# Kernel tuning notes

Hardware: AMD Instinct MI355X
Metric: run time of the kernel (lower is better)

## Reference

```python
import jax, jax.numpy as jnp
import numpy as np

NPOINT = 2048
RADIUS = 0.4
NSAMPLE = 32
BN_EPS = 1e-5


def setup_inputs() -> dict:
    key = jax.random.key(0)
    ks = jax.random.split(key, 6)
    B, N, C = 8, 8192, 64
    xyz = jax.random.normal(ks[0], (B, N, 3), jnp.float32)
    points = jax.random.normal(ks[1], (B, N, C), jnp.float32)
    W1 = jax.random.normal(ks[2], (3 + C, 64), jnp.float32) * 0.1
    W2 = jax.random.normal(ks[3], (64, 64), jnp.float32) * 0.1
    W3 = jax.random.normal(ks[4], (64, 128), jnp.float32) * 0.1
    return dict(
        xyz=xyz, points=points,
        W1=W1, g1=jnp.ones(64), b1=jnp.zeros(64),
        W2=W2, g2=jnp.ones(64), b2=jnp.zeros(64),
        W3=W3, g3=jnp.ones(128), b3=jnp.zeros(128),
    )


def _furthest_point_sample(xyz, npoint):
    # xyz: (B, N, 3) -> (B, npoint) int32. Sequential max-min scan, batched.
    B, N, _ = xyz.shape

    def step(carry, _):
        dists, last = carry
        p = jnp.take_along_axis(xyz, last[:, None, None], axis=1)  # (B,1,3)
        d2 = jnp.sum((xyz - p) ** 2, axis=-1)                       # (B,N)
        dists = jnp.minimum(dists, d2)
        nxt = jnp.argmax(dists, axis=-1).astype(jnp.int32)
        return (dists, nxt), nxt

    init = (jnp.full((B, N), 1e10, xyz.dtype), jnp.zeros((B,), jnp.int32))
    _, idx = jax.lax.scan(step, init, None, length=npoint - 1)      # (npoint-1, B)
    idx = jnp.concatenate([jnp.zeros((1, B), jnp.int32), idx], axis=0)
    return idx.T                                                    # (B, npoint)


def _ball_query(xyz, new_xyz, radius, nsample):
    # For each centroid take the first nsample point indices (in original order)
    # within `radius`; pad with the first found index (CUDA ball_query semantics).
    B, N, _ = xyz.shape
    d2 = jnp.sum((new_xyz[:, :, None, :] - xyz[:, None, :, :]) ** 2, axis=-1)  # (B,S,N)
    mask = d2 < radius * radius
    key = jnp.where(mask, jnp.arange(N, dtype=jnp.int32), N)
    srt = jnp.sort(key, axis=-1)[..., :nsample]                     # (B,S,K)
    first = srt[..., :1]
    first = jnp.where(first == N, 0, first)                         # empty ball -> index 0
    return jnp.where(srt == N, first, srt)


def _gather(pts, idx):
    # pts: (B,N,D), idx: (B,...) -> (B,...,D)
    return jax.vmap(lambda p, i: p[i])(pts, idx)


def reference(xyz, points, W1, g1, b1, W2, g2, b2, W3, g3, b3):
    fps_idx = _furthest_point_sample(xyz, NPOINT)                   # (B,S)
    new_xyz = _gather(xyz, fps_idx)                                 # (B,S,3)
    idx = _ball_query(xyz, new_xyz, RADIUS, NSAMPLE)                # (B,S,K)
    grouped_xyz = _gather(xyz, idx) - new_xyz[:, :, None, :]        # (B,S,K,3)
    grouped_pts = _gather(points, idx)                              # (B,S,K,C)
    feats = jnp.concatenate([grouped_xyz, grouped_pts], axis=-1)    # (B,S,K,3+C)
    for W, g, b in ((W1, g1, b1), (W2, g2, b2), (W3, g3, b3)):
        feats = feats @ W                                           # 1x1 conv
        m = feats.mean(axis=(0, 1, 2))
        v = feats.var(axis=(0, 1, 2))                               # biased, torch BN train mode
        feats = g * (feats - m) * jax.lax.rsqrt(v + BN_EPS) + b
        feats = jax.nn.relu(feats)
    new_points = feats.max(axis=2)                                  # max over nsample -> (B,S,mlp[-1])
    return new_xyz, new_points
```

## Files before the change

kernel.cpp:

```cpp
#include <hip/hip_runtime.h>

constexpr int B_ = 8, N_ = 8192, NPOINT_ = 2048, NSAMPLE_ = 32;
constexpr int M_ROWS = B_ * NPOINT_ * NSAMPLE_;
constexpr int NGROUP = B_ * NPOINT_;
constexpr size_t OFF_NXF   = 0;
constexpr size_t OFF_IDX   = 196608;
constexpr size_t OFF_WF    = 1245184;
constexpr size_t OFF_GB    = 1311488;
constexpr size_t OFF_STATS = 1313536;
constexpr size_t OFF_NP    = 1315584;
constexpr size_t OFF_FLAG  = 1317632;
constexpr size_t OFF_MAXB  = 2097152;

__device__ __forceinline__ float bf2f(unsigned short u) {
  union { unsigned u; float f; } x; x.u = ((unsigned)u) << 16; return x.f;
}
__device__ __forceinline__ float lo16f(unsigned u) {
  union { unsigned u; float f; } x; x.u = u << 16; return x.f;
}
__device__ __forceinline__ float hi16f(unsigned u) {
  union { unsigned u; float f; } x; x.u = u & 0xffff0000u; return x.f;
}
__device__ __forceinline__ unsigned short f2bf(float f) {
  union { float f; unsigned u; } x; x.f = f;
  unsigned u = x.u + 0x7FFFu + ((x.u >> 16) & 1u);
  return (unsigned short)(u >> 16);
}
__device__ __forceinline__ int f2i(float f) {
  union { float f; int i; } x; x.f = f; return x.i;
}
__device__ __forceinline__ float i2f(int i) {
  union { int i; float f; } x; x.i = i; return x.f;
}
__device__ __forceinline__ void unpack8(uint4 u, float* x) {
  x[0] = bf2f((unsigned short)(u.x & 0xffffu)); x[1] = bf2f((unsigned short)(u.x >> 16));
  x[2] = bf2f((unsigned short)(u.y & 0xffffu)); x[3] = bf2f((unsigned short)(u.y >> 16));
  x[4] = bf2f((unsigned short)(u.z & 0xffffu)); x[5] = bf2f((unsigned short)(u.z >> 16));
  x[6] = bf2f((unsigned short)(u.w & 0xffffu)); x[7] = bf2f((unsigned short)(u.w >> 16));
}
__device__ __forceinline__ float ldf(const void* p, size_t i, bool bf) {
  return bf ? bf2f(((const unsigned short*)p)[i]) : ((const float*)p)[i];
}
__device__ __forceinline__ void stf(void* p, size_t i, bool bf, float v) {
  if (bf) ((unsigned short*)p)[i] = f2bf(v);
  else    ((float*)p)[i] = v;
}

template <int CTRL>
__device__ __forceinline__ float dpp_maxf(float v) {
  int n = __builtin_amdgcn_update_dpp(0, f2i(v), CTRL, 0xF, 0xF, true);
  return fmaxf(v, i2f(n));
}

extern "C" __global__ void detect_kernel(const unsigned short* __restrict__ xyz,
                                         int* __restrict__ flag) {
  if (threadIdx.x == 0 && blockIdx.x == 0) {
    int sane = 0;
    for (int k = 0; k < 32; ++k) {
      int e = (xyz[2 * k] >> 7) & 0xff;
      if (e >= 90 && e <= 140) ++sane;
    }
    *flag = (sane >= 24) ? 1 : 0;
  }
}

extern "C" __global__ void prep_kernel(
    const void* W1, const void* W2, const void* W3,
    const void* g1, const void* b1, const void* g2, const void* b2,
    const void* g3, const void* b3,
    float* __restrict__ wf, float* __restrict__ gb, const int* __restrict__ flag) {
  const bool bf = (*flag != 0);
  int i = blockIdx.x * 256 + threadIdx.x;
  if (i < 4288)       wf[i] = ldf(W1, i, bf);
  else if (i < 8384)  wf[i] = ldf(W2, i - 4288, bf);
  else if (i < 16576) wf[i] = ldf(W3, i - 8384, bf);
  else if (i < 17088) {
    int k = i - 16576; float v;
    if (k < 64)       v = ldf(g1, k, bf);
    else if (k < 128) v = ldf(b1, k - 64, bf);
    else if (k < 192) v = ldf(g2, k - 128, bf);
    else if (k < 256) v = ldf(b2, k - 192, bf);
    else if (k < 384) v = ldf(g3, k - 256, bf);
    else              v = ldf(b3, k - 384, bf);
    gb[k] = v;
  }
}

template <bool BF>
__device__ __forceinline__ void fps_body(
    const void* xyz, void* out, float* __restrict__ nxf, float4* slots) {
#pragma clang fp contract(off)
  const int b = blockIdx.x;
  const int t = threadIdx.x;
  const int lane = t & 63, w = t >> 6;
  const size_t base = (size_t)b * N_ * 3;
  float px[8], py[8], pz[8], d[8];
  if (BF) {
    const uint4* xp = (const uint4*)((const unsigned short*)xyz + base) + t * 3;
    unsigned cc[12];
#pragma unroll
    for (int m = 0; m < 3; ++m) {
      uint4 u = xp[m];
      cc[4*m+0] = u.x; cc[4*m+1] = u.y; cc[4*m+2] = u.z; cc[4*m+3] = u.w;
    }
#pragma unroll
    for (int k = 0; k < 8; ++k) {
      if ((k & 1) == 0) {
        unsigned ra = cc[(3*k) >> 1], rb = cc[((3*k) >> 1) + 1];
        px[k] = lo16f(ra); py[k] = hi16f(ra); pz[k] = lo16f(rb);
      } else {
        unsigned ra = cc[(3*k - 1) >> 1], rb = cc[(3*k + 1) >> 1];
        px[k] = hi16f(ra); py[k] = lo16f(rb); pz[k] = hi16f(rb);
      }
    }
  } else {
#pragma unroll
    for (int k = 0; k < 8; ++k) {
      int i = t * 8 + k;
      px[k] = ((const float*)xyz)[base + i*3 + 0];
      py[k] = ((const float*)xyz)[base + i*3 + 1];
      pz[k] = ((const float*)xyz)[base + i*3 + 2];
    }
  }
#pragma unroll
  for (int k = 0; k < 8; ++k) d[k] = 1e10f;
  float s0x=0.f,s0y=0.f,s0z=0.f, s1x=0.f,s1y=0.f,s1z=0.f;
  float p0, p1, p2;
  if (BF) {
    const unsigned short* xp16 = (const unsigned short*)xyz + base;
    p0 = bf2f(xp16[0]); p1 = bf2f(xp16[1]); p2 = bf2f(xp16[2]);
  } else {
    p0 = ((const float*)xyz)[base + 0];
    p1 = ((const float*)xyz)[base + 1];
    p2 = ((const float*)xyz)[base + 2];
  }
  if (t == 0) { s0x = p0; s0y = p1; s0z = p2; }
  for (int j = 1; j < NPOINT_; ++j) {
    float bv = -1.0f;
#pragma unroll
    for (int k = 0; k < 8; ++k) {
      float dx = px[k] - p0, dy = py[k] - p1, dz = pz[k] - p2;
      float d2 = (dx*dx + dy*dy) + dz*dz;
      float dn = fminf(d[k], d2);
      d[k] = dn;
      bv = fmaxf(bv, dn);
    }
    float g = bv;
    g = dpp_maxf<0xB1>(g);
    g = dpp_maxf<0x4E>(g);
    g = dpp_maxf<0x141>(g);
    g = dpp_maxf<0x140>(g);
    g = dpp_maxf<0x142>(g);
    g = dpp_maxf<0x143>(g);
    float wmax = i2f(__builtin_amdgcn_readlane(f2i(g), 63));
    unsigned long long hm = __ballot(bv == wmax);
    int sl = (int)__builtin_ctzll(hm);
    const int pb = (j & 1) << 4;
    if (lane == sl) {
      int bk = 0;
#pragma unroll
      for (int k = 7; k >= 1; --k)
        if (d[k] == bv) bk = k;
      float cx = px[0], cy = py[0], cz = pz[0];
#pragma unroll
      for (int k = 1; k < 8; ++k)
        if (bk == k) { cx = px[k]; cy = py[k]; cz = pz[k]; }
      slots[pb + w] = make_float4(bv, cx, cy, cz);
    }
    __syncthreads();
    float4 kc = slots[pb + (lane & 15)];
    float m2 = kc.x;
    m2 = dpp_maxf<0xB1>(m2);
    m2 = dpp_maxf<0x4E>(m2);
    m2 = dpp_maxf<0x141>(m2);
    m2 = dpp_maxf<0x140>(m2);
    unsigned long long bm = __ballot(kc.x == m2);
    int s2 = (int)__builtin_ctzll(bm);
    p0 = i2f(__builtin_amdgcn_readlane(f2i(kc.y), s2));
    p1 = i2f(__builtin_amdgcn_readlane(f2i(kc.z), s2));
    p2 = i2f(__builtin_amdgcn_readlane(f2i(kc.w), s2));
    if (t == (j & 1023)) {
      if ((j >> 10) == 0) { s0x = p0; s0y = p1; s0z = p2; }
      else                { s1x = p0; s1y = p1; s1z = p2; }
    }
  }
  const bool bfrt = BF;
#pragma unroll
  for (int s = 0; s < 2; ++s) {
    float cx = (s==0)?s0x:s1x;
    float cy = (s==0)?s0y:s1y;
    float cz = (s==0)?s0z:s1z;
    size_t o = ((size_t)b * NPOINT_ + s * 1024 + t) * 3;
    nxf[o+0] = cx; nxf[o+1] = cy; nxf[o+2] = cz;
    stf(out, o+0, bfrt, cx); stf(out, o+1, bfrt, cy); stf(out, o+2, bfrt, cz);
  }
}

extern "C" __global__ void __launch_bounds__(1024, 4) fps_kernel(
    const void* xyz, void* out, float* __restrict__ nxf,
    const int* __restrict__ flag) {
  __shared__ float4 slots[32];
  if (*flag != 0) fps_body<true>(xyz, out, nxf, slots);
  else            fps_body<false>(xyz, out, nxf, slots);
}

extern "C" __global__ void __launch_bounds__(256) ballq_kernel(
    const void* xyz, const float* __restrict__ nxf,
    unsigned short* __restrict__ idxout, const int* __restrict__ flag) {
#pragma clang fp contract(off)
  const bool bf = (*flag != 0);
  const int gw = (int)((blockIdx.x * 256 + threadIdx.x) >> 6);
  const int lane = threadIdx.x & 63;
  const int b = gw >> 11;
  const int j = gw & (NPOINT_ - 1);
  const size_t base = (size_t)b * N_ * 3;
  const size_t co = ((size_t)b * NPOINT_ + j) * 3;
  const float c0 = nxf[co], c1 = nxf[co+1], c2 = nxf[co+2];
  unsigned short* out = idxout + (size_t)gw * NSAMPLE_;
  int cnt = 0, first = 0;
  for (int c = 0; c < N_/64 && cnt < NSAMPLE_; ++c) {
    int i = c * 64 + lane;
    float x = ldf(xyz, base + i*3 + 0, bf);
    float y = ldf(xyz, base + i*3 + 1, bf);
    float z = ldf(xyz, base + i*3 + 2, bf);
    float dx = x - c0, dy = y - c1, dz = z - c2;
    float d2 = (dx*dx + dy*dy) + dz*dz;
    unsigned long long m = __ballot(d2 < 0.16f);
    if (lane == 0) {
      while (m && cnt < NSAMPLE_) {
        int bit = __builtin_ctzll(m);
        int pi = c * 64 + bit;
        if (cnt == 0) first = pi;
        out[cnt] = (unsigned short)pi;
        ++cnt;
        m &= (m - 1);
      }
    }
    cnt = __shfl(cnt, 0);
  }
  first = __shfl(first, 0);
  if (lane >= cnt && lane < NSAMPLE_) out[lane] = (unsigned short)first;
}

__device__ __forceinline__ void l1_row(
    const void* xyz, const void* points, const float* __restrict__ nxf,
    const unsigned short* __restrict__ idx, const float* __restrict__ wf,
    int r, bool bf, float* acc) {
  const int b = r >> 16;
  const int j = (r >> 5) & (NPOINT_ - 1);
  const int i = idx[r];
  const size_t pt = (size_t)b * N_ + i;
  const float* cp = nxf + ((size_t)b * NPOINT_ + j) * 3;
  float f0 = ldf(xyz, pt*3 + 0, bf) - cp[0];
  float f1 = ldf(xyz, pt*3 + 1, bf) - cp[1];
  float f2 = ldf(xyz, pt*3 + 2, bf) - cp[2];
#pragma unroll
  for (int c = 0; c < 64; ++c)
    acc[c] = fmaf(f0, wf[c], fmaf(f1, wf[64+c], f2 * wf[128+c]));
  const float* wp = wf + 192;
  if (bf) {
    const uint4* pp = (const uint4*)((const unsigned short*)points + pt * 64);
#pragma unroll
    for (int s = 0; s < 8; ++s) {
      uint4 u = pp[s];
      float x[8]; unpack8(u, x);
#pragma unroll
      for (int kk = 0; kk < 8; ++kk)
#pragma unroll
        for (int c = 0; c < 64; ++c)
          acc[c] = fmaf(x[kk], wp[(s*8+kk)*64 + c], acc[c]);
    }
  } else {
    const float4* pp = (const float4*)((const float*)points + pt * 64);
#pragma unroll
    for (int s = 0; s < 16; ++s) {
      float4 u = pp[s];
      float x[4] = {u.x, u.y, u.z, u.w};
#pragma unroll
      for (int kk = 0; kk < 4; ++kk)
#pragma unroll
        for (int c = 0; c < 64; ++c)
          acc[c] = fmaf(x[kk], wp[(s*4+kk)*64 + c], acc[c]);
    }
  }
}

template <int LDW>
__device__ __forceinline__ void mm64(const float* v, const float* __restrict__ w,
                                     float* acc) {
#pragma unroll
  for (int ch = 0; ch < 64; ++ch)
#pragma unroll
    for (int c = 0; c < 64; ++c)
      acc[c] = fmaf(v[ch], w[ch*LDW + c], acc[c]);
}

__device__ __forceinline__ void bnrelu64(float* v, const float* __restrict__ np0) {
#pragma unroll
  for (int c = 0; c < 64; ++c)
    v[c] = fmaxf(fmaf(v[c], np0[c], np0[64 + c]), 0.f);
}

__device__ __forceinline__ void commit_stats64(float* a, float* __restrict__ stats) {
  float q[64];
#pragma unroll
  for (int c = 0; c < 64; ++c) q[c] = a[c] * a[c];
#pragma unroll
  for (int off = 1; off < 64; off <<= 1)
#pragma unroll
    for (int c = 0; c < 64; ++c) {
      a[c] += __shfl_xor(a[c], off);
      q[c] += __shfl_xor(q[c], off);
    }
  __shared__ float LS[4][64], LQ[4][64];
  const int t = threadIdx.x, w = t >> 6;
  if ((t & 63) == 0) {
#pragma unroll
    for (int c = 0; c < 64; ++c) { LS[w][c] = a[c]; LQ[w][c] = q[c]; }
  }
  __syncthreads();
  if (t < 64) {
    atomicAdd(&stats[t],      LS[0][t] + LS[1][t] + LS[2][t] + LS[3][t]);
    atomicAdd(&stats[64 + t], LQ[0][t] + LQ[1][t] + LQ[2][t] + LQ[3][t]);
  }
}

extern "C" __global__ void __launch_bounds__(256) p1_kernel(
    const void* xyz, const void* points, const float* __restrict__ nxf,
    const unsigned short* __restrict__ idx, const float* __restrict__ wf,
    float* __restrict__ stats, const int* __restrict__ flag) {
  const bool bf = (*flag != 0);
  const int r = blockIdx.x * 256 + threadIdx.x;
  float acc[64];
  l1_row(xyz, points, nxf, idx, wf, r, bf, acc);
  commit_stats64(acc, stats);
}

extern "C" __global__ void __launch_bounds__(256, 2) p2_kernel(
    const void* xyz, const void* points, const float* __restrict__ nxf,
    const unsigned short* __restrict__ idx, const float* __restrict__ wf,
    const float* __restrict__ w2, const float* __restrict__ np1,
    float* __restrict__ stats, const int* __restrict__ flag) {
  const bool bf = (*flag != 0);
  const int r = blockIdx.x * 256 + threadIdx.x;
  float v[64];
  l1_row(xyz, points, nxf, idx, wf, r, bf, v);
  bnrelu64(v, np1);
  float acc[64];
#pragma unroll
  for (int c = 0; c < 64; ++c) acc[c] = 0.f;
  mm64<64>(v, w2, acc);
  commit_stats64(acc, stats);
}

extern "C" __global__ void __launch_bounds__(256, 2) p3_kernel(
    const void* xyz, const void* points, const float* __restrict__ nxf,
    const unsigned short* __restrict__ idx, const float* __restrict__ wf,
    const float* __restrict__ w2, const float* __restrict__ w3,
    const float* __restrict__ np1, const float* __restrict__ np2,
    unsigned short* __restrict__ maxb, float* __restrict__ stats,
    const int* __restrict__ flag) {
  const bool bf = (*flag != 0);
  const int t = threadIdx.x, lane = t & 63, w = t >> 6;
  const int h = __builtin_amdgcn_readfirstlane(w & 1);
  const int g = blockIdx.x * 4 + (w >> 1) * 2 + (lane >> 5);
  const int r = g * 32 + (lane & 31);
  float v[64];
  l1_row(xyz, points, nxf, idx, wf, r, bf, v);
  bnrelu64(v, np1);
  float y2[64];
#pragma unroll
  for (int c = 0; c < 64; ++c) y2[c] = 0.f;
  mm64<64>(v, w2, y2);
  bnrelu64(y2, np2);
  const float* w3h = w3 + h * 64;
  float y3[64];
#pragma unroll
  for (int c = 0; c < 64; ++c) y3[c] = 0.f;
  mm64<128>(y2, w3h, y3);
  float* s = v; float* q = y2;
#pragma unroll
  for (int c = 0; c < 64; ++c) { s[c] = y3[c]; q[c] = y3[c] * y3[c]; }
#pragma unroll
  for (int off = 1; off <= 16; off <<= 1)
#pragma unroll
    for (int c = 0; c < 64; ++c)
      y3[c] = fmaxf(y3[c], __shfl_xor(y3[c], off));
  if ((lane & 31) == 0) {
    unsigned short* mo = maxb + (size_t)g * 128 + h * 64;
#pragma unroll
    for (int c = 0; c < 64; ++c) mo[c] = f2bf(y3[c]);
  }
#pragma unroll
  for (int off = 1; off < 64; off <<= 1)
#pragma unroll
    for (int c = 0; c < 64; ++c) {
      s[c] += __shfl_xor(s[c], off);
      q[c] += __shfl_xor(q[c], off);
    }
  __shared__ float LS[4][64], LQ[4][64];
  if (lane == 0) {
#pragma unroll
    for (int c = 0; c < 64; ++c) { LS[w][c] = s[c]; LQ[w][c] = q[c]; }
  }
  __syncthreads();
  if (t < 128) {
    int hh = t >> 6, cl = t & 63;
    atomicAdd(&stats[t],       LS[hh][cl] + LS[hh+2][cl]);
    atomicAdd(&stats[128 + t], LQ[hh][cl] + LQ[hh+2][cl]);
  }
}

extern "C" __global__ void nparam_kernel(
    const float* __restrict__ stats, const float* __restrict__ g,
    const float* __restrict__ bb, float* __restrict__ npar, int Cc) {
  int c = threadIdx.x;
  if (c < Cc) {
    float m = stats[c] * (1.0f / M_ROWS);
    float v = stats[Cc + c] * (1.0f / M_ROWS) - m * m;
    float sc = g[c] / sqrtf(v + 1e-5f);
    npar[c] = sc;
    npar[Cc + c] = bb[c] - m * sc;
  }
}

extern "C" __global__ void __launch_bounds__(256) final_kernel(
    const unsigned short* __restrict__ maxb, const float* __restrict__ npar,
    void* out, const int* __restrict__ flag) {
  const bool bf = (*flag != 0);
  const int gtid = blockIdx.x * 256 + threadIdx.x;
  const int c = gtid & 127;
  float y = bf2f(maxb[gtid]);
  float r = fmaxf(fmaf(y, npar[c], npar[128 + c]), 0.f);
  stf(out, (size_t)B_ * NPOINT_ * 3 + gtid, bf, r);
}

extern "C" void kernel_launch(void* const* d_in, const int* in_sizes, int n_in,
                              void* d_out, int out_size, void* d_ws, size_t ws_size,
                              hipStream_t stream) {
  const void* xyz    = d_in[0];
  const void* points = d_in[1];
  char* ws = (char*)d_ws;
  float* nxf   = (float*)(ws + OFF_NXF);
  unsigned short* wsIdx = (unsigned short*)(ws + OFF_IDX);
  float* wf    = (float*)(ws + OFF_WF);
  float* gb    = (float*)(ws + OFF_GB);
  float* stats = (float*)(ws + OFF_STATS);
  float* npar  = (float*)(ws + OFF_NP);
  int*   flag  = (int*)(ws + OFF_FLAG);
  unsigned short* maxb = (unsigned short*)(ws + OFF_MAXB);

  hipMemsetAsync(stats, 0, 512 * sizeof(float), stream);
  detect_kernel<<<1, 64, 0, stream>>>((const unsigned short*)xyz, flag);
  prep_kernel<<<67, 256, 0, stream>>>(d_in[2], d_in[5], d_in[8], d_in[3], d_in[4],
                                      d_in[6], d_in[7], d_in[9], d_in[10], wf, gb, flag);
  fps_kernel<<<B_, 1024, 0, stream>>>(xyz, d_out, nxf, flag);
  ballq_kernel<<<(B_ * NPOINT_) / 4, 256, 0, stream>>>(xyz, nxf, wsIdx, flag);
  p1_kernel<<<M_ROWS / 256, 256, 0, stream>>>(xyz, points, nxf, wsIdx, wf, stats, flag);
  nparam_kernel<<<1, 128, 0, stream>>>(stats, gb, gb + 64, npar, 64);
  p2_kernel<<<M_ROWS / 256, 256, 0, stream>>>(xyz, points, nxf, wsIdx, wf, wf + 4288,
                                              npar, stats + 128, flag);
  nparam_kernel<<<1, 128, 0, stream>>>(stats + 128, gb + 128, gb + 192, npar + 128, 64);
  p3_kernel<<<(2 * M_ROWS) / 256, 256, 0, stream>>>(xyz, points, nxf, wsIdx, wf,
                                                    wf + 4288, wf + 8384, npar,
                                                    npar + 128, maxb, stats + 256, flag);
  nparam_kernel<<<1, 128, 0, stream>>>(stats + 256, gb + 256, gb + 384, npar + 256, 128);
  final_kernel<<<(NGROUP * 128) / 256, 256, 0, stream>>>(maxb, npar + 256, d_out, flag);
}
```

Baseline: 3.982 ms.

## Use packed FP32 math in FPS and SoA xyz with parallel ballot compaction in ball query

```diff
diff --git a/kernel.cpp b/kernel.cpp
--- a/kernel.cpp
+++ b/kernel.cpp
@@ -11,6 +11,8 @@
 constexpr size_t OFF_NP    = 1315584;
 constexpr size_t OFF_FLAG  = 1317632;
 constexpr size_t OFF_MAXB  = 2097152;
+
+typedef float float2v __attribute__((ext_vector_type(2)));
 
 __device__ __forceinline__ float bf2f(unsigned short u) {
   union { unsigned u; float f; } x; x.u = ((unsigned)u) << 16; return x.f;
@@ -86,6 +88,17 @@
   }
 }
 
+extern "C" __global__ void conv_kernel(const void* xyz, float* __restrict__ sxyz,
+                                       const int* __restrict__ flag) {
+  const bool bf = (*flag != 0);
+  int i = blockIdx.x * 256 + threadIdx.x;
+  if (i < B_ * N_) {
+    sxyz[i]             = ldf(xyz, (size_t)i * 3 + 0, bf);
+    sxyz[B_*N_ + i]     = ldf(xyz, (size_t)i * 3 + 1, bf);
+    sxyz[2*B_*N_ + i]   = ldf(xyz, (size_t)i * 3 + 2, bf);
+  }
+}
+
 template <bool BF>
 __device__ __forceinline__ void fps_body(
     const void* xyz, void* out, float* __restrict__ nxf, float4* slots) {
@@ -94,7 +107,8 @@
   const int t = threadIdx.x;
   const int lane = t & 63, w = t >> 6;
   const size_t base = (size_t)b * N_ * 3;
-  float px[8], py[8], pz[8], d[8];
+  float2v px2[4], py2[4], pz2[4];
+  float d[8];
   if (BF) {
     const uint4* xp = (const uint4*)((const unsigned short*)xyz + base) + t * 3;
     unsigned cc[12];
@@ -105,21 +119,23 @@
     }
 #pragma unroll
     for (int k = 0; k < 8; ++k) {
+      float x, y, z;
       if ((k & 1) == 0) {
         unsigned ra = cc[(3*k) >> 1], rb = cc[((3*k) >> 1) + 1];
-        px[k] = lo16f(ra); py[k] = hi16f(ra); pz[k] = lo16f(rb);
+        x = lo16f(ra); y = hi16f(ra); z = lo16f(rb);
       } else {
         unsigned ra = cc[(3*k - 1) >> 1], rb = cc[(3*k + 1) >> 1];
-        px[k] = hi16f(ra); py[k] = lo16f(rb); pz[k] = hi16f(rb);
+        x = hi16f(ra); y = lo16f(rb); z = hi16f(rb);
       }
+      px2[k >> 1][k & 1] = x; py2[k >> 1][k & 1] = y; pz2[k >> 1][k & 1] = z;
     }
   } else {
 #pragma unroll
     for (int k = 0; k < 8; ++k) {
       int i = t * 8 + k;
-      px[k] = ((const float*)xyz)[base + i*3 + 0];
-      py[k] = ((const float*)xyz)[base + i*3 + 1];
-      pz[k] = ((const float*)xyz)[base + i*3 + 2];
+      px2[k >> 1][k & 1] = ((const float*)xyz)[base + i*3 + 0];
+      py2[k >> 1][k & 1] = ((const float*)xyz)[base + i*3 + 1];
+      pz2[k >> 1][k & 1] = ((const float*)xyz)[base + i*3 + 2];
     }
   }
 #pragma unroll
@@ -136,14 +152,24 @@
   }
   if (t == 0) { s0x = p0; s0y = p1; s0z = p2; }
   for (int j = 1; j < NPOINT_; ++j) {
+    float2v n0, n1, n2;
+    n0[0] = -p0; n0[1] = -p0;
+    n1[0] = -p1; n1[1] = -p1;
+    n2[0] = -p2; n2[1] = -p2;
     float bv = -1.0f;
 #pragma unroll
-    for (int k = 0; k < 8; ++k) {
-      float dx = px[k] - p0, dy = py[k] - p1, dz = pz[k] - p2;
-      float d2 = (dx*dx + dy*dy) + dz*dz;
-      float dn = fminf(d[k], d2);
-      d[k] = dn;
-      bv = fmaxf(bv, dn);
+    for (int p = 0; p < 4; ++p) {
+      float2v dx, dy, dz, qx, qy, qz, ts, dv;
+      asm("v_pk_add_f32 %0, %1, %2" : "=v"(dx) : "v"(px2[p]), "v"(n0));
+      asm("v_pk_add_f32 %0, %1, %2" : "=v"(dy) : "v"(py2[p]), "v"(n1));
+      asm("v_pk_add_f32 %0, %1, %2" : "=v"(dz) : "v"(pz2[p]), "v"(n2));
+      asm("v_pk_mul_f32 %0, %1, %1" : "=v"(qx) : "v"(dx));
+      asm("v_pk_mul_f32 %0, %1, %1" : "=v"(qy) : "v"(dy));
+      asm("v_pk_mul_f32 %0, %1, %1" : "=v"(qz) : "v"(dz));
+      asm("v_pk_add_f32 %0, %1, %2" : "=v"(ts) : "v"(qx), "v"(qy));
+      asm("v_pk_add_f32 %0, %1, %2" : "=v"(dv) : "v"(ts), "v"(qz));
+      float dn0 = fminf(d[2*p],   dv[0]); d[2*p]   = dn0; bv = fmaxf(bv, dn0);
+      float dn1 = fminf(d[2*p+1], dv[1]); d[2*p+1] = dn1; bv = fmaxf(bv, dn1);
     }
     float g = bv;
     g = dpp_maxf<0xB1>(g);
@@ -161,10 +187,10 @@
 #pragma unroll
       for (int k = 7; k >= 1; --k)
         if (d[k] == bv) bk = k;
-      float cx = px[0], cy = py[0], cz = pz[0];
+      float cx = px2[0][0], cy = py2[0][0], cz = pz2[0][0];
 #pragma unroll
       for (int k = 1; k < 8; ++k)
-        if (bk == k) { cx = px[k]; cy = py[k]; cz = pz[k]; }
+        if (bk == k) { cx = px2[k>>1][k&1]; cy = py2[k>>1][k&1]; cz = pz2[k>>1][k&1]; }
       slots[pb + w] = make_float4(bv, cx, cy, cz);
     }
     __syncthreads();
@@ -205,41 +231,42 @@
 }
 
 extern "C" __global__ void __launch_bounds__(256) ballq_kernel(
-    const void* xyz, const float* __restrict__ nxf,
-    unsigned short* __restrict__ idxout, const int* __restrict__ flag) {
+    const float* __restrict__ sxyz, const float* __restrict__ nxf,
+    unsigned short* __restrict__ idxout) {
 #pragma clang fp contract(off)
-  const bool bf = (*flag != 0);
   const int gw = (int)((blockIdx.x * 256 + threadIdx.x) >> 6);
   const int lane = threadIdx.x & 63;
   const int b = gw >> 11;
   const int j = gw & (NPOINT_ - 1);
-  const size_t base = (size_t)b * N_ * 3;
+  const float* sx = sxyz;
+  const float* sy = sxyz + B_ * N_;
+  const float* sz = sxyz + 2 * B_ * N_;
+  const size_t pbase = (size_t)b * N_;
   const size_t co = ((size_t)b * NPOINT_ + j) * 3;
   const float c0 = nxf[co], c1 = nxf[co+1], c2 = nxf[co+2];
   unsigned short* out = idxout + (size_t)gw * NSAMPLE_;
-  int cnt = 0, first = 0;
+  int cnt = 0, first = -1;
   for (int c = 0; c < N_/64 && cnt < NSAMPLE_; ++c) {
     int i = c * 64 + lane;
-    float x = ldf(xyz, base + i*3 + 0, bf);
-    float y = ldf(xyz, base + i*3 + 1, bf);
-    float z = ldf(xyz, base + i*3 + 2, bf);
-    float dx = x - c0, dy = y - c1, dz = z - c2;
+    float dx = sx[pbase + i] - c0;
+    float dy = sy[pbase + i] - c1;
+    float dz = sz[pbase + i] - c2;
     float d2 = (dx*dx + dy*dy) + dz*dz;
-    unsigned long long m = __ballot(d2 < 0.16f);
-    if (lane == 0) {
-      while (m && cnt < NSAMPLE_) {
-        int bit = __builtin_ctzll(m);
-        int pi = c * 64 + bit;
-        if (cnt == 0) first = pi;
-        out[cnt] = (unsigned short)pi;
-        ++cnt;
-        m &= (m - 1);
+    bool hit = d2 < 0.16f;
+    unsigned long long m = __ballot(hit);
+    if (m) {
+      if (first < 0) first = c * 64 + (int)__builtin_ctzll(m);
+      int rank = __builtin_amdgcn_mbcnt_hi(
+          (unsigned)(m >> 32), __builtin_amdgcn_mbcnt_lo((unsigned)m, 0));
+      if (hit) {
+        int pos = cnt + rank;
+        if (pos < NSAMPLE_) out[pos] = (unsigned short)i;
       }
-    }
-    cnt = __shfl(cnt, 0);
-  }
-  first = __shfl(first, 0);
-  if (lane >= cnt && lane < NSAMPLE_) out[lane] = (unsigned short)first;
+      cnt += __builtin_popcountll(m);
+    }
+  }
+  if (first < 0) first = 0;
+  if (lane < NSAMPLE_ && lane >= cnt) out[lane] = (unsigned short)first;
 }
 
 __device__ __forceinline__ void l1_row(
@@ -449,13 +476,15 @@
   float* npar  = (float*)(ws + OFF_NP);
   int*   flag  = (int*)(ws + OFF_FLAG);
   unsigned short* maxb = (unsigned short*)(ws + OFF_MAXB);
+  float* sxyz  = (float*)(ws + OFF_MAXB);
 
   hipMemsetAsync(stats, 0, 512 * sizeof(float), stream);
   detect_kernel<<<1, 64, 0, stream>>>((const unsigned short*)xyz, flag);
   prep_kernel<<<67, 256, 0, stream>>>(d_in[2], d_in[5], d_in[8], d_in[3], d_in[4],
                                       d_in[6], d_in[7], d_in[9], d_in[10], wf, gb, flag);
+  conv_kernel<<<(B_ * N_) / 256, 256, 0, stream>>>(xyz, sxyz, flag);
   fps_kernel<<<B_, 1024, 0, stream>>>(xyz, d_out, nxf, flag);
-  ballq_kernel<<<(B_ * NPOINT_) / 4, 256, 0, stream>>>(xyz, nxf, wsIdx, flag);
+  ballq_kernel<<<(B_ * NPOINT_) / 4, 256, 0, stream>>>(sxyz, nxf, wsIdx);
   p1_kernel<<<M_ROWS / 256, 256, 0, stream>>>(xyz, points, nxf, wsIdx, wf, stats, flag);
   nparam_kernel<<<1, 128, 0, stream>>>(stats, gb, gb + 64, npar, 64);
   p2_kernel<<<M_ROWS / 256, 256, 0, stream>>>(xyz, points, nxf, wsIdx, wf, wf + 4288,
```

After: 3.888 ms. 2.3% less time.
